# Optimization experiments

Hardware: AMD Instinct MI355X
Metric: run time of the kernel (lower is better)

The kernel has to match this reference:

```python
import jax, jax.numpy as jnp
import numpy as np

N = 50000
E = 800000
HIDDEN = 128
NUM_HEADS = 8
D_HEAD = HIDDEN // NUM_HEADS


def setup_inputs() -> dict:
    key = jax.random.key(0)
    ks = jax.random.split(key, 12)
    sc = 1.0 / np.sqrt(HIDDEN)
    inp = {
        "h": jax.random.normal(ks[0], (N, HIDDEN), dtype=jnp.float32),
        "rows": jax.random.randint(ks[1], (E,), 0, N, dtype=jnp.int32),
        "cols": jax.random.randint(ks[2], (E,), 0, N, dtype=jnp.int32),
        "Wq": jax.random.normal(ks[3], (HIDDEN, HIDDEN), dtype=jnp.float32) * sc,
        "bq": jax.random.normal(ks[4], (HIDDEN,), dtype=jnp.float32) * sc,
        "Wk": jax.random.normal(ks[5], (HIDDEN, HIDDEN), dtype=jnp.float32) * sc,
        "bk": jax.random.normal(ks[6], (HIDDEN,), dtype=jnp.float32) * sc,
        "Wv": jax.random.normal(ks[7], (HIDDEN, HIDDEN), dtype=jnp.float32) * sc,
        "bv": jax.random.normal(ks[8], (HIDDEN,), dtype=jnp.float32) * sc,
        "Wo": jax.random.normal(ks[9], (HIDDEN, HIDDEN), dtype=jnp.float32) * sc,
        "bo": jax.random.normal(ks[10], (HIDDEN,), dtype=jnp.float32) * sc,
    }
    return inp


def reference(h, rows, cols, Wq, bq, Wk, bk, Wv, bv, Wo, bo):
    n = h.shape[0]
    scaling = D_HEAD ** (-0.5)
    # projections; torch-style reshape splits hidden as (d_head, num_heads)
    q = ((h @ Wq.T + bq).reshape(n, D_HEAD, NUM_HEADS)) * scaling
    k = (h @ Wk.T + bk).reshape(n, D_HEAD, NUM_HEADS)
    v = (h @ Wv.T + bv).reshape(n, D_HEAD, NUM_HEADS)
    # SDDMM: per-edge, per-head score = q[row] . k[col]   -> [E, H]
    scores = jnp.einsum("edh,edh->eh", q[rows], k[cols])
    # row-wise (destination) stable softmax over variable-degree neighborhoods
    m = jax.ops.segment_max(scores, rows, num_segments=n)  # [N, H]
    e = jnp.exp(scores - m[rows])
    s = jax.ops.segment_sum(e, rows, num_segments=n)  # [N, H]
    attn = e / s[rows]  # [E, H]
    # SpMM: out[i] = sum_{(i,j) in E} attn[e] * v[j]
    out = jax.ops.segment_sum(attn[:, None, :] * v[cols], rows, num_segments=n)
    return out.reshape(n, HIDDEN) @ Wo.T + bo
```

## Files before the change

### kernel.cpp

```cpp
#include <hip/hip_runtime.h>
#include <math.h>

#define N_NODES 50000
#define N_EDGES 800000
#define HID 128
#define CAP 64
#define ROWBLK 782
#define CVT_H_TASKS (N_NODES * HID / 4)
#define CVT_TASKS   (CVT_H_TASKS + 4 * 4096)

typedef __bf16 bf16_t;
typedef bf16_t bf16x8 __attribute__((ext_vector_type(8)));
typedef float  f32x4  __attribute__((ext_vector_type(4)));

__device__ __forceinline__ ushort f2b(float x) {
    union { bf16_t b; ushort u; } c;
    c.b = (bf16_t)x;
    return c.u;
}

__global__ __launch_bounds__(256) void prep_build(
    const float* __restrict__ h,
    const float* __restrict__ Wq, const float* __restrict__ Wk,
    const float* __restrict__ Wv, const float* __restrict__ Wo,
    ushort* __restrict__ hb,
    ushort* __restrict__ wq, ushort* __restrict__ wk,
    ushort* __restrict__ wv, ushort* __restrict__ wo,
    const int* __restrict__ rows, const int* __restrict__ cols,
    int* __restrict__ cnt, ushort* __restrict__ slots)
{
    const int t = blockIdx.x * 256 + threadIdx.x;

    if (t < N_EDGES) {
        int r = rows[t];
        int p = atomicAdd(&cnt[r], 1);
        if (p < CAP) slots[r * CAP + p] = (ushort)cols[t];
    }
    if (t < CVT_TASKS) {
        const float* src;
        ushort* dst;
        int i;
        if (t < CVT_H_TASKS) { src = h; dst = hb; i = t; }
        else {
            int wt = t - CVT_H_TASKS;
            int w  = wt >> 12;
            i = wt & 4095;
            src = (w == 0) ? Wq : (w == 1) ? Wk : (w == 2) ? Wv : Wo;
            dst = (w == 0) ? wq : (w == 1) ? wk : (w == 2) ? wv : wo;
        }
        float4 f = ((const float4*)src)[i];
        ushort4 o;
        o.x = f2b(f.x); o.y = f2b(f.y); o.z = f2b(f.z); o.w = f2b(f.w);
        ((ushort4*)dst)[i] = o;
    }
}

template <int PHASE>
__global__ __launch_bounds__(256) void gemm16(
    const ushort* __restrict__ A,
    const ushort* __restrict__ w0, const ushort* __restrict__ w1,
    const ushort* __restrict__ w2,
    const float* __restrict__ b0, const float* __restrict__ b1,
    const float* __restrict__ b2,
    uint* __restrict__ qp, uint2* __restrict__ kv,
    float* __restrict__ outf)
{
    const int lane = threadIdx.x & 63;
    const int wv   = threadIdx.x >> 6;
    const int mrow = lane & 15;
    const int quad = lane >> 4;
    const int rb   = blockIdx.x * 64;
    const int mat  = (PHASE == 0) ? blockIdx.y : 3;

    const ushort* W    = (mat == 1) ? w1 : (mat == 2) ? w2 : w0;
    const float*  bias = (mat == 1) ? b1 : (mat == 2) ? b2 : b0;

    const int c0 = wv * 32 + mrow;
    const int c1 = c0 + 16;

    bf16x8 bfr[2][4];
#pragma unroll
    for (int kc = 0; kc < 4; ++kc) {
        bfr[0][kc] = *(const bf16x8*)(W + c0 * HID + kc * 32 + quad * 8);
        bfr[1][kc] = *(const bf16x8*)(W + c1 * HID + kc * 32 + quad * 8);
    }

    f32x4 acc[4][2];
#pragma unroll
    for (int s = 0; s < 4; ++s) {
        acc[s][0] = (f32x4){0.f, 0.f, 0.f, 0.f};
        acc[s][1] = (f32x4){0.f, 0.f, 0.f, 0.f};
    }

#pragma unroll
    for (int s = 0; s < 4; ++s) {
        const int r0 = rb + s * 16;
        if (r0 >= N_NODES) break;
        const ushort* ap = A + (size_t)(r0 + mrow) * HID + quad * 8;
        bf16x8 a0 = *(const bf16x8*)(ap);
        bf16x8 a1 = *(const bf16x8*)(ap + 32);
        bf16x8 a2 = *(const bf16x8*)(ap + 64);
        bf16x8 a3 = *(const bf16x8*)(ap + 96);
        acc[s][0] = __builtin_amdgcn_mfma_f32_16x16x32_bf16(a0, bfr[0][0], acc[s][0], 0, 0, 0);
        acc[s][1] = __builtin_amdgcn_mfma_f32_16x16x32_bf16(a0, bfr[1][0], acc[s][1], 0, 0, 0);
        acc[s][0] = __builtin_amdgcn_mfma_f32_16x16x32_bf16(a1, bfr[0][1], acc[s][0], 0, 0, 0);
        acc[s][1] = __builtin_amdgcn_mfma_f32_16x16x32_bf16(a1, bfr[1][1], acc[s][1], 0, 0, 0);
        acc[s][0] = __builtin_amdgcn_mfma_f32_16x16x32_bf16(a2, bfr[0][2], acc[s][0], 0, 0, 0);
        acc[s][1] = __builtin_amdgcn_mfma_f32_16x16x32_bf16(a2, bfr[1][2], acc[s][1], 0, 0, 0);
        acc[s][0] = __builtin_amdgcn_mfma_f32_16x16x32_bf16(a3, bfr[0][3], acc[s][0], 0, 0, 0);
        acc[s][1] = __builtin_amdgcn_mfma_f32_16x16x32_bf16(a3, bfr[1][3], acc[s][1], 0, 0, 0);
    }

#pragma unroll
    for (int t = 0; t < 2; ++t) {
        const int   c    = (t == 0) ? c0 : c1;
        const float bc   = bias[c];
        const int   p    = 8 * (c >> 4) + (c & 7);
        const int   half = (c >> 3) & 1;
#pragma unroll
        for (int s = 0; s < 4; ++s) {
            if (rb + s * 16 >= N_NODES) break;
#pragma unroll
            for (int r = 0; r < 4; ++r) {
                const int orow = rb + s * 16 + quad * 4 + r;
                const float val = acc[s][t][r] + bc;
                if (PHASE == 1) {
                    outf[(size_t)orow * HID + c] = val;
                } else if (mat == 0) {
                    ((ushort*)qp)[((size_t)orow * 64 + p) * 2 + half] = f2b(val * 0.25f);
                } else if (mat == 1) {
                    ((ushort*)kv)[((size_t)orow * 64 + p) * 4 + half] = f2b(val);
                } else {
                    ((ushort*)kv)[((size_t)orow * 64 + p) * 4 + 2 + half] = f2b(val);
                }
            }
        }
    }
}

__device__ __forceinline__ void edge_acc(uint2 rr, float q0, float q1,
                                         float& l, float& Oa, float& Ob)
{
    float k0 = __uint_as_float(rr.x << 16);
    float k1 = __uint_as_float(rr.x & 0xffff0000u);
    float p = q0 * k0 + q1 * k1;
    p += __shfl_xor(p, 8);
    p += __shfl_xor(p, 16);
    p += __shfl_xor(p, 32);
    float ex = __expf(fminf(p, 80.f));
    l  += ex;
    Oa += ex * __uint_as_float(rr.y << 16);
    Ob += ex * __uint_as_float(rr.y & 0xffff0000u);
}

__global__ __launch_bounds__(256) void attn_fused(
    const uint* __restrict__ qp, const uint2* __restrict__ kv,
    const int* __restrict__ cnt, const ushort* __restrict__ slots,
    ushort* __restrict__ ao)
{
    const int lane = threadIdx.x & 63;
    const int node = blockIdx.x * 4 + (threadIdx.x >> 6);
    if (node >= N_NODES) return;

    const uint qraw = qp[(size_t)node * 64 + lane];
    const float q0 = __uint_as_float(qraw << 16);
    const float q1 = __uint_as_float(qraw & 0xffff0000u);

    int deg = cnt[node];
    if (deg > CAP) deg = CAP;
    const int myslot = (lane < deg) ? (int)slots[(size_t)node * CAP + lane] : 0;

    float ls[4] = {0.f, 0.f, 0.f, 0.f};
    float Oa[4] = {0.f, 0.f, 0.f, 0.f};
    float Ob[4] = {0.f, 0.f, 0.f, 0.f};

    int j = 0;
    for (; j + 4 <= deg; j += 4) {
        int s0 = __shfl(myslot, j);
        int s1 = __shfl(myslot, j + 1);
        int s2 = __shfl(myslot, j + 2);
        int s3 = __shfl(myslot, j + 3);
        uint2 r0 = kv[(size_t)s0 * 64 + lane];
        uint2 r1 = kv[(size_t)s1 * 64 + lane];
        uint2 r2 = kv[(size_t)s2 * 64 + lane];
        uint2 r3 = kv[(size_t)s3 * 64 + lane];
        edge_acc(r0, q0, q1, ls[0], Oa[0], Ob[0]);
        edge_acc(r1, q0, q1, ls[1], Oa[1], Ob[1]);
        edge_acc(r2, q0, q1, ls[2], Oa[2], Ob[2]);
        edge_acc(r3, q0, q1, ls[3], Oa[3], Ob[3]);
    }
    for (; j < deg; ++j) {
        int s = __shfl(myslot, j);
        uint2 rr = kv[(size_t)s * 64 + lane];
        edge_acc(rr, q0, q1, ls[0], Oa[0], Ob[0]);
    }

    const float l  = (ls[0] + ls[1]) + (ls[2] + ls[3]);
    const float O0 = (Oa[0] + Oa[1]) + (Oa[2] + Oa[3]);
    const float O1 = (Ob[0] + Ob[1]) + (Ob[2] + Ob[3]);
    const float inv = (l > 0.f) ? 1.f / l : 0.f;

    const int ce = 16 * (lane >> 3) + (lane & 7);
    ao[(size_t)node * HID + ce]     = f2b(O0 * inv);
    ao[(size_t)node * HID + ce + 8] = f2b(O1 * inv);
}

extern "C" void kernel_launch(void* const* d_in, const int* in_sizes, int n_in,
                              void* d_out, int out_size, void* d_ws, size_t ws_size,
                              hipStream_t stream)
{
    const float* h    = (const float*)d_in[0];
    const int*   rows = (const int*)  d_in[1];
    const int*   cols = (const int*)  d_in[2];
    const float* Wq   = (const float*)d_in[3];
    const float* bq   = (const float*)d_in[4];
    const float* Wk   = (const float*)d_in[5];
    const float* bk   = (const float*)d_in[6];
    const float* Wv   = (const float*)d_in[7];
    const float* bv   = (const float*)d_in[8];
    const float* Wo   = (const float*)d_in[9];
    const float* bo   = (const float*)d_in[10];
    float* out = (float*)d_out;

    char* ws = (char*)d_ws;
    uint*   qp    = (uint*)ws;    ws += (size_t)N_NODES * 64 * 4;
    uint2*  kv    = (uint2*)ws;   ws += (size_t)N_NODES * 64 * 8;
    ushort* hb    = (ushort*)ws;  ws += (size_t)N_NODES * HID * 2;
    ushort* aob   = (ushort*)ws;  ws += (size_t)N_NODES * HID * 2;
    ushort* wqb   = (ushort*)ws;  ws += 128 * 128 * 2;
    ushort* wkb   = (ushort*)ws;  ws += 128 * 128 * 2;
    ushort* wvb   = (ushort*)ws;  ws += 128 * 128 * 2;
    ushort* wob   = (ushort*)ws;  ws += 128 * 128 * 2;
    int*    cnt   = (int*)ws;     ws += (size_t)N_NODES * 4;
    ushort* slots = (ushort*)ws;

    hipMemsetAsync(cnt, 0, N_NODES * sizeof(int), stream);

    dim3 blk(256);
    prep_build<<<(CVT_TASKS + 255) / 256, blk, 0, stream>>>(
        h, Wq, Wk, Wv, Wo, hb, wqb, wkb, wvb, wob, rows, cols, cnt, slots);

    gemm16<0><<<dim3(ROWBLK, 3), blk, 0, stream>>>(
        hb, wqb, wkb, wvb, bq, bk, bv, qp, kv, nullptr);

    attn_fused<<<(N_NODES + 3) / 4, blk, 0, stream>>>(qp, kv, cnt, slots, aob);

    gemm16<1><<<dim3(ROWBLK, 1), blk, 0, stream>>>(
        aob, wob, wob, wob, bo, bo, bo, qp, kv, out);
}
```

Measured before the change: 243.9 us.

## Fuse h conversion into QKV GEMM and widen attention edge unroll to eight

The separate pass that converts h to bf16 is dropped. The QKV GEMM now reads fp32 h directly, converts it in registers, and reuses that A tile across all three weight matrices in one block, so the bf16 copy of h is no longer written and re-read. The attention kernel loads eight neighbour rows per iteration with predication instead of four plus a scalar tail, giving more memory-level parallelism. The costs are more registers and some wasted loads on the padded tail edges.

```diff
diff --git a/kernel.cpp b/kernel.cpp
--- a/kernel.cpp
+++ b/kernel.cpp
@@ -5,9 +5,8 @@
 #define N_EDGES 800000
 #define HID 128
 #define CAP 64
-#define ROWBLK 782
-#define CVT_H_TASKS (N_NODES * HID / 4)
-#define CVT_TASKS   (CVT_H_TASKS + 4 * 4096)
+#define GQ_GRID ((N_NODES + 31) / 32)
+#define GO_GRID ((N_NODES + 63) / 64)
 
 typedef __bf16 bf16_t;
 typedef bf16_t bf16x8 __attribute__((ext_vector_type(8)));
@@ -19,11 +18,9 @@
     return c.u;
 }
 
-__global__ __launch_bounds__(256) void prep_build(
-    const float* __restrict__ h,
+__global__ __launch_bounds__(256) void prep(
     const float* __restrict__ Wq, const float* __restrict__ Wk,
     const float* __restrict__ Wv, const float* __restrict__ Wo,
-    ushort* __restrict__ hb,
     ushort* __restrict__ wq, ushort* __restrict__ wk,
     ushort* __restrict__ wv, ushort* __restrict__ wo,
     const int* __restrict__ rows, const int* __restrict__ cols,
@@ -31,51 +28,198 @@
 {
     const int t = blockIdx.x * 256 + threadIdx.x;
 
+    if (t < 4 * 4096) {
+        int w = t >> 12, i = t & 4095;
+        const float* src = (w == 0) ? Wq : (w == 1) ? Wk : (w == 2) ? Wv : Wo;
+        ushort*      dst = (w == 0) ? wq : (w == 1) ? wk : (w == 2) ? wv : wo;
+        float4 f = ((const float4*)src)[i];
+        ushort4 o;
+        o.x = f2b(f.x); o.y = f2b(f.y); o.z = f2b(f.z); o.w = f2b(f.w);
+        ((ushort4*)dst)[i] = o;
+    }
     if (t < N_EDGES) {
         int r = rows[t];
         int p = atomicAdd(&cnt[r], 1);
         if (p < CAP) slots[r * CAP + p] = (ushort)cols[t];
     }
-    if (t < CVT_TASKS) {
-        const float* src;
-        ushort* dst;
-        int i;
-        if (t < CVT_H_TASKS) { src = h; dst = hb; i = t; }
-        else {
-            int wt = t - CVT_H_TASKS;
-            int w  = wt >> 12;
-            i = wt & 4095;
-            src = (w == 0) ? Wq : (w == 1) ? Wk : (w == 2) ? Wv : Wo;
-            dst = (w == 0) ? wq : (w == 1) ? wk : (w == 2) ? wv : wo;
-        }
-        float4 f = ((const float4*)src)[i];
-        ushort4 o;
-        o.x = f2b(f.x); o.y = f2b(f.y); o.z = f2b(f.z); o.w = f2b(f.w);
-        ((ushort4*)dst)[i] = o;
-    }
-}
-
-template <int PHASE>
-__global__ __launch_bounds__(256) void gemm16(
-    const ushort* __restrict__ A,
-    const ushort* __restrict__ w0, const ushort* __restrict__ w1,
-    const ushort* __restrict__ w2,
-    const float* __restrict__ b0, const float* __restrict__ b1,
-    const float* __restrict__ b2,
-    uint* __restrict__ qp, uint2* __restrict__ kv,
-    float* __restrict__ outf)
+}
+
+__global__ __launch_bounds__(256) void gemm_qkv(
+    const float* __restrict__ h,
+    const ushort* __restrict__ wqm, const ushort* __restrict__ wkm,
+    const ushort* __restrict__ wvm,
+    const float* __restrict__ bq, const float* __restrict__ bk,
+    const float* __restrict__ bv,
+    uint* __restrict__ qp, uint2* __restrict__ kv)
 {
     const int lane = threadIdx.x & 63;
-    const int wv   = threadIdx.x >> 6;
+    const int wid  = threadIdx.x >> 6;
+    const int mrow = lane & 15;
+    const int quad = lane >> 4;
+    const int rb   = blockIdx.x * 32;
+
+    bf16x8 a[2][4];
+#pragma unroll
+    for (int s = 0; s < 2; ++s) {
+        if (rb + s * 16 >= N_NODES) break;
+        const float* src = h + (size_t)(rb + s * 16 + mrow) * HID + quad * 8;
+#pragma unroll
+        for (int kc = 0; kc < 4; ++kc) {
+            float4 f0 = *(const float4*)(src + kc * 32);
+            float4 f1 = *(const float4*)(src + kc * 32 + 4);
+            bf16x8 tb;
+            tb[0] = (bf16_t)f0.x; tb[1] = (bf16_t)f0.y;
+            tb[2] = (bf16_t)f0.z; tb[3] = (bf16_t)f0.w;
+            tb[4] = (bf16_t)f1.x; tb[5] = (bf16_t)f1.y;
+            tb[6] = (bf16_t)f1.z; tb[7] = (bf16_t)f1.w;
+            a[s][kc] = tb;
+        }
+    }
+
+    const int c0   = wid * 32 + mrow;
+    const int c1   = c0 + 16;
+    const int p0   = 16 * wid + (mrow & 7);
+    const int half = mrow >> 3;
+
+    bf16x8 bfr[2][4];
+    f32x4  acc[2][2];
+
+#define LOAD_B(W)                                                          \
+    _Pragma("unroll")                                                      \
+    for (int kc = 0; kc < 4; ++kc) {                                       \
+        bfr[0][kc] = *(const bf16x8*)((W) + c0 * HID + kc * 32 + quad * 8);\
+        bfr[1][kc] = *(const bf16x8*)((W) + c1 * HID + kc * 32 + quad * 8);\
+    }
+#define RUN_MFMA(dst)                                                      \
+    _Pragma("unroll")                                                      \
+    for (int s = 0; s < 2; ++s) {                                          \
+        dst[s][0] = (f32x4){0.f, 0.f, 0.f, 0.f};                           \
+        dst[s][1] = (f32x4){0.f, 0.f, 0.f, 0.f};                           \
+        if (rb + s * 16 >= N_NODES) continue;                              \
+        _Pragma("unroll")                                                  \
+        for (int kc = 0; kc < 4; ++kc) {                                   \
+            dst[s][0] = __builtin_amdgcn_mfma_f32_16x16x32_bf16(           \
+                a[s][kc], bfr[0][kc], dst[s][0], 0, 0, 0);                 \
+            dst[s][1] = __builtin_amdgcn_mfma_f32_16x16x32_bf16(           \
+                a[s][kc], bfr[1][kc], dst[s][1], 0, 0, 0);                 \
+        }                                                                  \
+    }
+
+    LOAD_B(wqm);
+    RUN_MFMA(acc);
+    {
+        const float b0 = bq[c0], b1 = bq[c1];
+        ushort* qps = (ushort*)qp;
+#pragma unroll
+        for (int s = 0; s < 2; ++s) {
+            if (rb + s * 16 >= N_NODES) break;
+#pragma unroll
+            for (int r = 0; r < 4; ++r) {
+                const size_t orow = rb + s * 16 + quad * 4 + r;
+                qps[((orow * 64 + p0) << 1) + half]     = f2b((acc[s][0][r] + b0) * 0.25f);
+                qps[((orow * 64 + p0 + 8) << 1) + half] = f2b((acc[s][1][r] + b1) * 0.25f);
+            }
+        }
+    }
+
+    f32x4 acck[2][2];
+    LOAD_B(wkm);
+    RUN_MFMA(acck);
+    LOAD_B(wvm);
+    RUN_MFMA(acc);
+
+    {
+        const float bk0 = bk[c0], bk1 = bk[c1];
+        const float bv0 = bv[c0], bv1 = bv[c1];
+        ushort* kvs = (ushort*)kv;
+#pragma unroll
+        for (int s = 0; s < 2; ++s) {
+            if (rb + s * 16 >= N_NODES) break;
+#pragma unroll
+            for (int r = 0; r < 4; ++r) {
+                const size_t orow = rb + s * 16 + quad * 4 + r;
+                const size_t b0a = (orow * 64 + p0) << 2;
+                const size_t b1a = (orow * 64 + p0 + 8) << 2;
+                kvs[b0a + half]     = f2b(acck[s][0][r] + bk0);
+                kvs[b1a + half]     = f2b(acck[s][1][r] + bk1);
+                kvs[b0a + 2 + half] = f2b(acc[s][0][r] + bv0);
+                kvs[b1a + 2 + half] = f2b(acc[s][1][r] + bv1);
+            }
+        }
+    }
+#undef LOAD_B
+#undef RUN_MFMA
+}
+
+__global__ __launch_bounds__(256) void attn_fused(
+    const uint* __restrict__ qp, const uint2* __restrict__ kv,
+    const int* __restrict__ cnt, const ushort* __restrict__ slots,
+    ushort* __restrict__ ao)
+{
+    const int lane = threadIdx.x & 63;
+    const int node = blockIdx.x * 4 + (threadIdx.x >> 6);
+    if (node >= N_NODES) return;
+
+    const uint qraw = qp[(size_t)node * 64 + lane];
+    const float q0 = __uint_as_float(qraw << 16);
+    const float q1 = __uint_as_float(qraw & 0xffff0000u);
+
+    int deg = cnt[node];
+    if (deg > CAP) deg = CAP;
+    const int myslot = (lane < deg) ? (int)slots[(size_t)node * CAP + lane] : 0;
+
+    float ls[8] = {0,0,0,0,0,0,0,0};
+    float Oa[8] = {0,0,0,0,0,0,0,0};
+    float Ob[8] = {0,0,0,0,0,0,0,0};
+
+    for (int base = 0; base < deg; base += 8) {
+        int sj[8];
+#pragma unroll
+        for (int u = 0; u < 8; ++u) {
+            int j  = base + u;
+            int jj = (j < deg) ? j : 0;
+            sj[u] = __shfl(myslot, jj);
+        }
+        uint2 rr[8];
+#pragma unroll
+        for (int u = 0; u < 8; ++u)
+            rr[u] = kv[(size_t)sj[u] * 64 + lane];
+#pragma unroll
+        for (int u = 0; u < 8; ++u) {
+            float k0 = __uint_as_float(rr[u].x << 16);
+            float k1 = __uint_as_float(rr[u].x & 0xffff0000u);
+            float p = q0 * k0 + q1 * k1;
+            p += __shfl_xor(p, 8);
+            p += __shfl_xor(p, 16);
+            p += __shfl_xor(p, 32);
+            float ex = (base + u < deg) ? __expf(fminf(p, 80.f)) : 0.f;
+            ls[u] += ex;
+            Oa[u] += ex * __uint_as_float(rr[u].y << 16);
+            Ob[u] += ex * __uint_as_float(rr[u].y & 0xffff0000u);
+        }
+    }
+
+    const float l  = ((ls[0] + ls[1]) + (ls[2] + ls[3])) + ((ls[4] + ls[5]) + (ls[6] + ls[7]));
+    const float O0 = ((Oa[0] + Oa[1]) + (Oa[2] + Oa[3])) + ((Oa[4] + Oa[5]) + (Oa[6] + Oa[7]));
+    const float O1 = ((Ob[0] + Ob[1]) + (Ob[2] + Ob[3])) + ((Ob[4] + Ob[5]) + (Ob[6] + Ob[7]));
+    const float inv = (l > 0.f) ? 1.f / l : 0.f;
+
+    const int ce = 16 * (lane >> 3) + (lane & 7);
+    ao[(size_t)node * HID + ce]     = f2b(O0 * inv);
+    ao[(size_t)node * HID + ce + 8] = f2b(O1 * inv);
+}
+
+__global__ __launch_bounds__(256) void gemm_out(
+    const ushort* __restrict__ A, const ushort* __restrict__ W,
+    const float* __restrict__ bias, float* __restrict__ out)
+{
+    const int lane = threadIdx.x & 63;
+    const int wid  = threadIdx.x >> 6;
     const int mrow = lane & 15;
     const int quad = lane >> 4;
     const int rb   = blockIdx.x * 64;
-    const int mat  = (PHASE == 0) ? blockIdx.y : 3;
-
-    const ushort* W    = (mat == 1) ? w1 : (mat == 2) ? w2 : w0;
-    const float*  bias = (mat == 1) ? b1 : (mat == 2) ? b2 : b0;
-
-    const int c0 = wv * 32 + mrow;
+
+    const int c0 = wid * 32 + mrow;
     const int c1 = c0 + 16;
 
     bf16x8 bfr[2][4];
@@ -94,9 +238,8 @@
 
 #pragma unroll
     for (int s = 0; s < 4; ++s) {
-        const int r0 = rb + s * 16;
-        if (r0 >= N_NODES) break;
-        const ushort* ap = A + (size_t)(r0 + mrow) * HID + quad * 8;
+        if (rb + s * 16 >= N_NODES) break;
+        const ushort* ap = A + (size_t)(rb + s * 16 + mrow) * HID + quad * 8;
         bf16x8 a0 = *(const bf16x8*)(ap);
         bf16x8 a1 = *(const bf16x8*)(ap + 32);
         bf16x8 a2 = *(const bf16x8*)(ap + 64);
@@ -113,96 +256,18 @@
 
 #pragma unroll
     for (int t = 0; t < 2; ++t) {
-        const int   c    = (t == 0) ? c0 : c1;
-        const float bc   = bias[c];
-        const int   p    = 8 * (c >> 4) + (c & 7);
-        const int   half = (c >> 3) & 1;
+        const int c = (t == 0) ? c0 : c1;
+        const float bc = bias[c];
 #pragma unroll
         for (int s = 0; s < 4; ++s) {
             if (rb + s * 16 >= N_NODES) break;
 #pragma unroll
             for (int r = 0; r < 4; ++r) {
-                const int orow = rb + s * 16 + quad * 4 + r;
-                const float val = acc[s][t][r] + bc;
-                if (PHASE == 1) {
-                    outf[(size_t)orow * HID + c] = val;
-                } else if (mat == 0) {
-                    ((ushort*)qp)[((size_t)orow * 64 + p) * 2 + half] = f2b(val * 0.25f);
-                } else if (mat == 1) {
-                    ((ushort*)kv)[((size_t)orow * 64 + p) * 4 + half] = f2b(val);
-                } else {
-                    ((ushort*)kv)[((size_t)orow * 64 + p) * 4 + 2 + half] = f2b(val);
-                }
+                const size_t orow = rb + s * 16 + quad * 4 + r;
+                out[orow * HID + c] = acc[s][t][r] + bc;
             }
         }
     }
-}
-
-__device__ __forceinline__ void edge_acc(uint2 rr, float q0, float q1,
-                                         float& l, float& Oa, float& Ob)
-{
-    float k0 = __uint_as_float(rr.x << 16);
-    float k1 = __uint_as_float(rr.x & 0xffff0000u);
-    float p = q0 * k0 + q1 * k1;
-    p += __shfl_xor(p, 8);
-    p += __shfl_xor(p, 16);
-    p += __shfl_xor(p, 32);
-    float ex = __expf(fminf(p, 80.f));
-    l  += ex;
-    Oa += ex * __uint_as_float(rr.y << 16);
-    Ob += ex * __uint_as_float(rr.y & 0xffff0000u);
-}
-
-__global__ __launch_bounds__(256) void attn_fused(
-    const uint* __restrict__ qp, const uint2* __restrict__ kv,
-    const int* __restrict__ cnt, const ushort* __restrict__ slots,
-    ushort* __restrict__ ao)
-{
-    const int lane = threadIdx.x & 63;
-    const int node = blockIdx.x * 4 + (threadIdx.x >> 6);
-    if (node >= N_NODES) return;
-
-    const uint qraw = qp[(size_t)node * 64 + lane];
-    const float q0 = __uint_as_float(qraw << 16);
-    const float q1 = __uint_as_float(qraw & 0xffff0000u);
-
-    int deg = cnt[node];
-    if (deg > CAP) deg = CAP;
-    const int myslot = (lane < deg) ? (int)slots[(size_t)node * CAP + lane] : 0;
-
-    float ls[4] = {0.f, 0.f, 0.f, 0.f};
-    float Oa[4] = {0.f, 0.f, 0.f, 0.f};
-    float Ob[4] = {0.f, 0.f, 0.f, 0.f};
-
-    int j = 0;
-    for (; j + 4 <= deg; j += 4) {
-        int s0 = __shfl(myslot, j);
-        int s1 = __shfl(myslot, j + 1);
-        int s2 = __shfl(myslot, j + 2);
-        int s3 = __shfl(myslot, j + 3);
-        uint2 r0 = kv[(size_t)s0 * 64 + lane];
-        uint2 r1 = kv[(size_t)s1 * 64 + lane];
-        uint2 r2 = kv[(size_t)s2 * 64 + lane];
-        uint2 r3 = kv[(size_t)s3 * 64 + lane];
-        edge_acc(r0, q0, q1, ls[0], Oa[0], Ob[0]);
-        edge_acc(r1, q0, q1, ls[1], Oa[1], Ob[1]);
-        edge_acc(r2, q0, q1, ls[2], Oa[2], Ob[2]);
-        edge_acc(r3, q0, q1, ls[3], Oa[3], Ob[3]);
-    }
-    for (; j < deg; ++j) {
-        int s = __shfl(myslot, j);
-        uint2 rr = kv[(size_t)s * 64 + lane];
-        edge_acc(rr, q0, q1, ls[0], Oa[0], Ob[0]);
-    }
-
-    const float l  = (ls[0] + ls[1]) + (ls[2] + ls[3]);
-    const float O0 = (Oa[0] + Oa[1]) + (Oa[2] + Oa[3]);
-    const float O1 = (Ob[0] + Ob[1]) + (Ob[2] + Ob[3]);
-    const float inv = (l > 0.f) ? 1.f / l : 0.f;
-
-    const int ce = 16 * (lane >> 3) + (lane & 7);
-    ao[(size_t)node * HID + ce]     = f2b(O0 * inv);
-    ao[(size_t)node * HID + ce + 8] = f2b(O1 * inv);
 }
 
 extern "C" void kernel_launch(void* const* d_in, const int* in_sizes, int n_in,
@@ -225,7 +290,6 @@
     char* ws = (char*)d_ws;
     uint*   qp    = (uint*)ws;    ws += (size_t)N_NODES * 64 * 4;
     uint2*  kv    = (uint2*)ws;   ws += (size_t)N_NODES * 64 * 8;
-    ushort* hb    = (ushort*)ws;  ws += (size_t)N_NODES * HID * 2;
     ushort* aob   = (ushort*)ws;  ws += (size_t)N_NODES * HID * 2;
     ushort* wqb   = (ushort*)ws;  ws += 128 * 128 * 2;
     ushort* wkb   = (ushort*)ws;  ws += 128 * 128 * 2;
@@ -237,14 +301,13 @@
     hipMemsetAsync(cnt, 0, N_NODES * sizeof(int), stream);
 
     dim3 blk(256);
-    prep_build<<<(CVT_TASKS + 255) / 256, blk, 0, stream>>>(
-        h, Wq, Wk, Wv, Wo, hb, wqb, wkb, wvb, wob, rows, cols, cnt, slots);
-
-    gemm16<0><<<dim3(ROWBLK, 3), blk, 0, stream>>>(
-        hb, wqb, wkb, wvb, bq, bk, bv, qp, kv, nullptr);
+    prep<<<(N_EDGES + 255) / 256, blk, 0, stream>>>(
+        Wq, Wk, Wv, Wo, wqb, wkb, wvb, wob, rows, cols, cnt, slots);
+
+    gemm_qkv<<<GQ_GRID, blk, 0, stream>>>(
+        h, wqb, wkb, wvb, bq, bk, bv, qp, kv);
 
     attn_fused<<<(N_NODES + 3) / 4, blk, 0, stream>>>(qp, kv, cnt, slots, aob);
 
-    gemm16<1><<<dim3(ROWBLK, 1), blk, 0, stream>>>(
-        aob, wob, wob, wob, bo, bo, bo, qp, kv, out);
-}
+    gemm_out<<<GO_GRID, blk, 0, stream>>>(aob, wob, bo, out);
+}
```

New measurement: 245.6 us. Within noise of the previous version (+0.7%).
